# Performance work log

Hardware: AMD Instinct MI355X
Metric: run time of the kernel (lower is better)

The kernel has to match this reference:

```python
import jax, jax.numpy as jnp
import numpy as np


def setup_inputs() -> dict:
    key = jax.random.key(0)
    k1, k2, k3 = jax.random.split(key, 3)
    G, E, C, H, I = 1, 8, 2048, 1024, 4096
    x = jax.random.normal(k1, (G, E, C, H), dtype=jnp.float32)
    # init per module.reset_parameters: normal std sqrt(0.1/hidden) and sqrt(0.1/intermediate)
    wi = jax.random.normal(k2, (E, H, I), dtype=jnp.float32) * np.sqrt(0.1 / H)
    wo = jax.random.normal(k3, (E, I, H), dtype=jnp.float32) * np.sqrt(0.1 / I)
    return {"x": x, "wi": wi, "wo": wo}


def reference(x, wi, wo):
    # x: [G, E, C, H] -> transpose to [E, G, C, H] -> [E, G*C, H]
    G, E, C, H = x.shape
    xt = jnp.swapaxes(x, 0, 1).reshape(E, G * C, H)
    # per-expert grouped GEMM: hidden -> intermediate, gelu, -> hidden
    h = jax.nn.gelu(jnp.einsum("eth,ehi->eti", xt, wi), approximate=False)
    out = jnp.einsum("eti,eih->eth", h, wo)
    out = out.reshape(E, G, C, H)
    return jnp.swapaxes(out, 0, 1)  # [G, E, C, H]
```

## Files before the change

kernel.cpp:

```cpp
#include <hip/hip_runtime.h>
#include <hip/hip_bf16.h>
#include <cstdint>

typedef __attribute__((ext_vector_type(4))) float f32x4;
typedef __attribute__((ext_vector_type(8))) short bf16x8;
typedef __attribute__((ext_vector_type(4))) short s16x4;
typedef __attribute__((ext_vector_type(8))) short s16x8;

__device__ __forceinline__ short f2bf(float f) {
    union { float f; unsigned u; } v; v.f = f;
    unsigned r = v.u + 0x7FFFu + ((v.u >> 16) & 1u);
    return (short)(r >> 16);
}

__global__ __launch_bounds__(256) void cast_bf16(const float* __restrict__ in,
                                                 short* __restrict__ out, long n) {
    long i = ((long)blockIdx.x * 256 + threadIdx.x) * 8;
    if (i + 7 < n) {
        float4 a = *(const float4*)(in + i);
        float4 b = *(const float4*)(in + i + 4);
        s16x8 o;
        o[0] = f2bf(a.x); o[1] = f2bf(a.y); o[2] = f2bf(a.z); o[3] = f2bf(a.w);
        o[4] = f2bf(b.x); o[5] = f2bf(b.y); o[6] = f2bf(b.z); o[7] = f2bf(b.w);
        *(s16x8*)(out + i) = o;
    }
}

__global__ __launch_bounds__(256) void transpose_cast(const float* __restrict__ in,
                                                      short* __restrict__ out,
                                                      int R, int C) {
    __shared__ float t[64][65];
    const size_t eoff = (size_t)blockIdx.z * R * C;
    in  += eoff;
    out += eoff;
    const int c0 = blockIdx.x * 64, r0 = blockIdx.y * 64;
    const int tid = threadIdx.x;
    const int rr  = tid >> 4;
    const int cc4 = (tid & 15) * 4;
    #pragma unroll
    for (int i = 0; i < 4; ++i) {
        const int row = i * 16 + rr;
        float4 v = *(const float4*)(in + (size_t)(r0 + row) * C + c0 + cc4);
        t[row][cc4 + 0] = v.x; t[row][cc4 + 1] = v.y;
        t[row][cc4 + 2] = v.z; t[row][cc4 + 3] = v.w;
    }
    __syncthreads();
    #pragma unroll
    for (int i = 0; i < 4; ++i) {
        const int oc = i * 16 + rr;
        s16x4 o;
        o[0] = f2bf(t[cc4 + 0][oc]);
        o[1] = f2bf(t[cc4 + 1][oc]);
        o[2] = f2bf(t[cc4 + 2][oc]);
        o[3] = f2bf(t[cc4 + 3][oc]);
        *(s16x4*)(out + (size_t)(c0 + oc) * R + r0 + cc4) = o;
    }
}

__device__ __forceinline__ void stage_tile64(const short* __restrict__ g,
                                             short* lds, int ld,
                                             int wave, int lane) {
    #pragma unroll
    for (int i = 0; i < 4; ++i) {
        const int c    = i * 256 + wave * 64 + lane;
        const int row  = c >> 3;
        const int slot = c & 7;
        const int gkc  = (slot ^ (row & 7)) << 3;
        const short* gp = g + (size_t)row * ld + gkc;
        short* lp = lds + (size_t)(i * 256 + wave * 64) * 8;
        __builtin_amdgcn_global_load_lds(
            (const __attribute__((address_space(1))) void*)gp,
            (__attribute__((address_space(3))) void*)lp, 16, 0, 0);
    }
}

template <int FUSE>
__global__ __launch_bounds__(256) void gemm_bt(const short* __restrict__ A,
                                               const short* __restrict__ Bt,
                                               void* __restrict__ Cout,
                                               int M, int N, int K) {
    __shared__ short As[128 * 64];
    __shared__ short Bs[128 * 64];
    const int tid  = threadIdx.x;
    const int lane = tid & 63;
    const int wave = tid >> 6;
    const int e    = blockIdx.z;
    A  += (size_t)e * M * K;
    Bt += (size_t)e * N * K;

    const int gridN = gridDim.x;
    const int lin   = blockIdx.y * gridN + blockIdx.x;
    const int band  = lin / (4 * gridN);
    const int rem   = lin - band * 4 * gridN;
    const int m0 = (band * 4 + (rem & 3)) * 128;
    const int n0 = (rem >> 2) * 128;

    const int wm = (wave >> 1) * 64;
    const int wn = (wave & 1) * 64;

    f32x4 acc[4][4] = {};

    const short* Ab = A  + (size_t)m0 * K;
    const short* Bb = Bt + (size_t)n0 * K;

    const int rA   = wm + (lane & 15);
    const int rB   = wn + (lane & 15);
    const int quad = lane >> 4;

    for (int k0 = 0; k0 < K; k0 += 64) {
        stage_tile64(Ab + k0, As, K, wave, lane);
        stage_tile64(Bb + k0, Bs, K, wave, lane);
        __syncthreads();

        #pragma unroll
        for (int s = 0; s < 2; ++s) {
            const int j = s * 4 + quad;
            bf16x8 af[4], bf[4];
            #pragma unroll
            for (int t = 0; t < 4; ++t) {
                const int ra = rA + t * 16;
                af[t] = *(const bf16x8*)&As[ra * 64 + ((j ^ (ra & 7)) << 3)];
            }
            #pragma unroll
            for (int t = 0; t < 4; ++t) {
                const int rb = rB + t * 16;
                bf[t] = *(const bf16x8*)&Bs[rb * 64 + ((j ^ (rb & 7)) << 3)];
            }
            #pragma unroll
            for (int i = 0; i < 4; ++i)
                #pragma unroll
                for (int jj = 0; jj < 4; ++jj)
                    acc[i][jj] = __builtin_amdgcn_mfma_f32_16x16x32_bf16(
                        af[i], bf[jj], acc[i][jj], 0, 0, 0);
        }
        __syncthreads();
    }

    const int r0 = quad << 2;
    const int cL = lane & 15;
    if (FUSE) {
        short* C = (short*)Cout + (size_t)e * M * N;
        #pragma unroll
        for (int i = 0; i < 4; ++i)
            #pragma unroll
            for (int j = 0; j < 4; ++j)
                #pragma unroll
                for (int r = 0; r < 4; ++r) {
                    const int row = m0 + wm + i * 16 + r0 + r;
                    const int col = n0 + wn + j * 16 + cL;
                    float v = acc[i][j][r];
                    v = 0.5f * v * (1.0f + erff(v * 0.70710678118654752f));
                    C[(size_t)row * N + col] = f2bf(v);
                }
    } else {
        float* C = (float*)Cout + (size_t)e * M * N;
        #pragma unroll
        for (int i = 0; i < 4; ++i)
            #pragma unroll
            for (int j = 0; j < 4; ++j)
                #pragma unroll
                for (int r = 0; r < 4; ++r) {
                    const int row = m0 + wm + i * 16 + r0 + r;
                    const int col = n0 + wn + j * 16 + cL;
                    C[(size_t)row * N + col] = acc[i][j][r];
                }
    }
}

extern "C" void kernel_launch(void* const* d_in, const int* in_sizes, int n_in,
                              void* d_out, int out_size, void* d_ws, size_t ws_size,
                              hipStream_t stream) {
    constexpr int E = 8, Ct = 2048, H = 1024, I = 4096;

    const float* x  = (const float*)d_in[0];
    const float* wi = (const float*)d_in[1];
    const float* wo = (const float*)d_in[2];
    float* out = (float*)d_out;

    char* ws = (char*)d_ws;
    short* xb  = (short*)(ws);
    short* wiT = (short*)(ws + (size_t)33554432);
    short* woT = (short*)(ws + (size_t)100663296);
    short* h   = (short*)(ws + (size_t)167772160);

    {
        long n = (long)E * Ct * H;
        cast_bf16<<<dim3((unsigned)(n / 2048)), dim3(256), 0, stream>>>(x, xb, n);
    }
    transpose_cast<<<dim3(I / 64, H / 64, E), dim3(256), 0, stream>>>(wi, wiT, H, I);
    transpose_cast<<<dim3(H / 64, I / 64, E), dim3(256), 0, stream>>>(wo, woT, I, H);

    gemm_bt<1><<<dim3(I / 128, Ct / 128, E), dim3(256), 0, stream>>>(
        xb, wiT, (void*)h, Ct, I, H);

    gemm_bt<0><<<dim3(H / 128, Ct / 128, E), dim3(256), 0, stream>>>(
        h, woT, (void*)out, Ct, H, I);
}
```

Measured before the change: 728.6 us.

## Rewrite GEMM as 256x256 tile with 4-stage LDS pipeline and 8 waves

Replaces the 128x128 single-buffered GEMM with a 256x256 tile, 512-thread kernel that uses a 4-deep ring of K=32 LDS stages. Loads are prefetched three stages ahead with explicit vmcnt waits and raw barriers, and MFMA phases run at raised priority. Tiles are remapped across XCDs with a chiplet-aware swizzle. The goal is to hide global-load latency, raise arithmetic intensity per LDS byte, and improve L2 locality. The cost is 128KB of LDS per block and tricky hand-written synchronisation.

```diff
diff --git a/kernel.cpp b/kernel.cpp
--- a/kernel.cpp
+++ b/kernel.cpp
@@ -57,112 +57,156 @@
     }
 }
 
-__device__ __forceinline__ void stage_tile64(const short* __restrict__ g,
-                                             short* lds, int ld,
-                                             int wave, int lane) {
-    #pragma unroll
-    for (int i = 0; i < 4; ++i) {
-        const int c    = i * 256 + wave * 64 + lane;
-        const int row  = c >> 3;
-        const int slot = c & 7;
-        const int gkc  = (slot ^ (row & 7)) << 3;
-        const short* gp = g + (size_t)row * ld + gkc;
-        short* lp = lds + (size_t)(i * 256 + wave * 64) * 8;
-        __builtin_amdgcn_global_load_lds(
-            (const __attribute__((address_space(1))) void*)gp,
-            (__attribute__((address_space(3))) void*)lp, 16, 0, 0);
-    }
+
+#define FENCE() asm volatile("" ::: "memory")
+#define BARRIER() do { FENCE(); __builtin_amdgcn_s_barrier(); FENCE(); } while (0)
+
+__device__ __forceinline__ void stage2(const short* g0, const short* g1, short* l0) {
+    __builtin_amdgcn_global_load_lds(
+        (const __attribute__((address_space(1))) void*)g0,
+        (__attribute__((address_space(3))) void*)l0, 16, 0, 0);
+    __builtin_amdgcn_global_load_lds(
+        (const __attribute__((address_space(1))) void*)g1,
+        (__attribute__((address_space(3))) void*)(l0 + 4096), 16, 0, 0);
 }
 
 template <int FUSE>
-__global__ __launch_bounds__(256) void gemm_bt(const short* __restrict__ A,
-                                               const short* __restrict__ Bt,
-                                               void* __restrict__ Cout,
-                                               int M, int N, int K) {
-    __shared__ short As[128 * 64];
-    __shared__ short Bs[128 * 64];
+__global__ __launch_bounds__(512, 2) void gemm_bt(const short* __restrict__ A,
+                                                  const short* __restrict__ Bt,
+                                                  void* __restrict__ Cout,
+                                                  int M, int N, int K) {
+    __shared__ short lds[65536];
     const int tid  = threadIdx.x;
     const int lane = tid & 63;
     const int wave = tid >> 6;
-    const int e    = blockIdx.z;
-    A  += (size_t)e * M * K;
-    Bt += (size_t)e * N * K;
-
-    const int gridN = gridDim.x;
-    const int lin   = blockIdx.y * gridN + blockIdx.x;
-    const int band  = lin / (4 * gridN);
-    const int rem   = lin - band * 4 * gridN;
-    const int m0 = (band * 4 + (rem & 3)) * 128;
-    const int n0 = (rem >> 2) * 128;
-
-    const int wm = (wave >> 1) * 64;
-    const int wn = (wave & 1) * 64;
-
-    f32x4 acc[4][4] = {};
-
-    const short* Ab = A  + (size_t)m0 * K;
-    const short* Bb = Bt + (size_t)n0 * K;
-
-    const int rA   = wm + (lane & 15);
-    const int rB   = wn + (lane & 15);
-    const int quad = lane >> 4;
-
-    for (int k0 = 0; k0 < K; k0 += 64) {
-        stage_tile64(Ab + k0, As, K, wave, lane);
-        stage_tile64(Bb + k0, Bs, K, wave, lane);
-        __syncthreads();
-
-        #pragma unroll
-        for (int s = 0; s < 2; ++s) {
-            const int j = s * 4 + quad;
-            bf16x8 af[4], bf[4];
-            #pragma unroll
-            for (int t = 0; t < 4; ++t) {
-                const int ra = rA + t * 16;
-                af[t] = *(const bf16x8*)&As[ra * 64 + ((j ^ (ra & 7)) << 3)];
-            }
-            #pragma unroll
-            for (int t = 0; t < 4; ++t) {
-                const int rb = rB + t * 16;
-                bf[t] = *(const bf16x8*)&Bs[rb * 64 + ((j ^ (rb & 7)) << 3)];
-            }
-            #pragma unroll
-            for (int i = 0; i < 4; ++i)
-                #pragma unroll
-                for (int jj = 0; jj < 4; ++jj)
-                    acc[i][jj] = __builtin_amdgcn_mfma_f32_16x16x32_bf16(
-                        af[i], bf[jj], acc[i][jj], 0, 0, 0);
+    const int wm   = wave >> 2;
+    const int wn   = wave & 3;
+
+    const int tilesM = M >> 8;
+    const int perE   = tilesM * (N >> 8);
+    const int total  = gridDim.x * gridDim.z;
+    int lin = blockIdx.z * gridDim.x + blockIdx.x;
+    lin = (lin & 7) * (total >> 3) + (lin >> 3);
+    const int e   = lin / perE;
+    const int rem = lin - e * perE;
+    const int m0  = (rem % tilesM) << 8;
+    const int n0  = (rem / tilesM) << 8;
+
+    const short* Ab = A  + (size_t)e * M * K + (size_t)m0 * K;
+    const short* Bb = Bt + (size_t)e * N * K + (size_t)n0 * K;
+
+    size_t goff[2];
+    #pragma unroll
+    for (int i = 0; i < 2; ++i) {
+        const int p  = i * 512 + tid;
+        const int r  = p >> 2;
+        const int sp = p & 3;
+        const int q  = sp ^ ((r >> 1) & 3);
+        goff[i] = (size_t)r * K + q * 8;
+    }
+    const int lwb = wave * 512;
+
+    const int lrow = lane & 15, lq = lane >> 4;
+    int offA[8], offB[4];
+    #pragma unroll
+    for (int m = 0; m < 8; ++m) {
+        const int r = wm * 128 + m * 16 + lrow;
+        offA[m] = (r * 4 + (lq ^ ((r >> 1) & 3))) * 8;
+    }
+    #pragma unroll
+    for (int n = 0; n < 4; ++n) {
+        const int r = wn * 64 + n * 16 + lrow;
+        offB[n] = (r * 4 + (lq ^ ((r >> 1) & 3))) * 8;
+    }
+
+    f32x4 acc[8][4] = {};
+    const int nk = K >> 5;
+
+    #pragma unroll
+    for (int t = 0; t < 3; ++t) {
+        const size_t k0 = (size_t)t * 32;
+        short* da = lds + (t & 3) * 8192 + lwb;
+        short* db = lds + 32768 + (t & 3) * 8192 + lwb;
+        stage2(Ab + k0 + goff[0], Ab + k0 + goff[1], da);
+        stage2(Bb + k0 + goff[0], Bb + k0 + goff[1], db);
+    }
+    asm volatile("s_waitcnt vmcnt(8)" ::: "memory");
+    BARRIER();
+
+    for (int t = 0; t < nk; ++t) {
+        const short* As = lds + (t & 3) * 8192;
+        const short* Bs = lds + 32768 + (t & 3) * 8192;
+        bf16x8 a0[4], b0[4], a1[4];
+
+        #pragma unroll
+        for (int m = 0; m < 4; ++m) a0[m] = *(const bf16x8*)(As + offA[m]);
+        #pragma unroll
+        for (int n = 0; n < 4; ++n) b0[n] = *(const bf16x8*)(Bs + offB[n]);
+        if (t + 3 < nk) {
+            const size_t k0 = (size_t)(t + 3) * 32;
+            stage2(Ab + k0 + goff[0], Ab + k0 + goff[1],
+                   lds + ((t + 3) & 3) * 8192 + lwb);
         }
-        __syncthreads();
-    }
-
-    const int r0 = quad << 2;
-    const int cL = lane & 15;
+        BARRIER();
+        __builtin_amdgcn_s_setprio(1);
+        #pragma unroll
+        for (int m = 0; m < 4; ++m)
+            #pragma unroll
+            for (int n = 0; n < 4; ++n)
+                acc[m][n] = __builtin_amdgcn_mfma_f32_16x16x32_bf16(
+                    a0[m], b0[n], acc[m][n], 0, 0, 0);
+        __builtin_amdgcn_s_setprio(0);
+        BARRIER();
+
+        #pragma unroll
+        for (int m = 0; m < 4; ++m) a1[m] = *(const bf16x8*)(As + offA[4 + m]);
+        if (t + 3 < nk) {
+            const size_t k0 = (size_t)(t + 3) * 32;
+            stage2(Bb + k0 + goff[0], Bb + k0 + goff[1],
+                   lds + 32768 + ((t + 3) & 3) * 8192 + lwb);
+        }
+        if (t < nk - 3)       asm volatile("s_waitcnt vmcnt(8)" ::: "memory");
+        else if (t == nk - 3) asm volatile("s_waitcnt vmcnt(4)" ::: "memory");
+        else if (t == nk - 2) asm volatile("s_waitcnt vmcnt(0)" ::: "memory");
+        BARRIER();
+        __builtin_amdgcn_s_setprio(1);
+        #pragma unroll
+        for (int m = 0; m < 4; ++m)
+            #pragma unroll
+            for (int n = 0; n < 4; ++n)
+                acc[4 + m][n] = __builtin_amdgcn_mfma_f32_16x16x32_bf16(
+                    a1[m], b0[n], acc[4 + m][n], 0, 0, 0);
+        __builtin_amdgcn_s_setprio(0);
+        BARRIER();
+    }
+
+    const int r0q = lq << 2;
+    const int cL  = lane & 15;
     if (FUSE) {
         short* C = (short*)Cout + (size_t)e * M * N;
         #pragma unroll
-        for (int i = 0; i < 4; ++i)
-            #pragma unroll
-            for (int j = 0; j < 4; ++j)
+        for (int m = 0; m < 8; ++m)
+            #pragma unroll
+            for (int n = 0; n < 4; ++n)
                 #pragma unroll
-                for (int r = 0; r < 4; ++r) {
-                    const int row = m0 + wm + i * 16 + r0 + r;
-                    const int col = n0 + wn + j * 16 + cL;
-                    float v = acc[i][j][r];
+                for (int rr = 0; rr < 4; ++rr) {
+                    const int row = m0 + wm * 128 + m * 16 + r0q + rr;
+                    const int col = n0 + wn * 64 + n * 16 + cL;
+                    float v = acc[m][n][rr];
                     v = 0.5f * v * (1.0f + erff(v * 0.70710678118654752f));
                     C[(size_t)row * N + col] = f2bf(v);
                 }
     } else {
         float* C = (float*)Cout + (size_t)e * M * N;
         #pragma unroll
-        for (int i = 0; i < 4; ++i)
-            #pragma unroll
-            for (int j = 0; j < 4; ++j)
+        for (int m = 0; m < 8; ++m)
+            #pragma unroll
+            for (int n = 0; n < 4; ++n)
                 #pragma unroll
-                for (int r = 0; r < 4; ++r) {
-                    const int row = m0 + wm + i * 16 + r0 + r;
-                    const int col = n0 + wn + j * 16 + cL;
-                    C[(size_t)row * N + col] = acc[i][j][r];
+                for (int rr = 0; rr < 4; ++rr) {
+                    const int row = m0 + wm * 128 + m * 16 + r0q + rr;
+                    const int col = n0 + wn * 64 + n * 16 + cL;
+                    C[(size_t)row * N + col] = acc[m][n][rr];
                 }
     }
 }
@@ -190,9 +234,7 @@
     transpose_cast<<<dim3(I / 64, H / 64, E), dim3(256), 0, stream>>>(wi, wiT, H, I);
     transpose_cast<<<dim3(H / 64, I / 64, E), dim3(256), 0, stream>>>(wo, woT, I, H);
 
-    gemm_bt<1><<<dim3(I / 128, Ct / 128, E), dim3(256), 0, stream>>>(
-        xb, wiT, (void*)h, Ct, I, H);
-
-    gemm_bt<0><<<dim3(H / 128, Ct / 128, E), dim3(256), 0, stream>>>(
-        h, woT, (void*)out, Ct, H, I);
-}
+    gemm_bt<1><<<dim3(128, 1, E), dim3(512), 0, stream>>>(xb, wiT, (void*)h, Ct, I, H);
+
+    gemm_bt<0><<<dim3(32, 1, E), dim3(512), 0, stream>>>(h, woT, (void*)out, Ct, H, I);
+}
```

Result: faster. 636.3 us (-12.7%).
